# Kernel tuning notes

Measured on AMD Instinct MI355X. Metric: run time of the kernel, lower is better.

## Reference

```python
import jax, jax.numpy as jnp
import numpy as np

GAMMA = 0.9
NUM_HEADS = 8
SCALE_BASE = 512.0
GN_EPS = 1e-5


def xpos(x):
    # Canonical RetNet XPOS rotary embedding (offset=0, downscale=False).
    B, S, D = x.shape
    half = D // 2
    scale_vec = (jnp.arange(0, D, 2, dtype=jnp.float32) + 0.4 * D) / (1.4 * D)  # [half]
    power = jnp.arange(S, dtype=jnp.float32) / SCALE_BASE                        # [S]
    scale = scale_vec[None, :] ** power[:, None]                                 # [S, half]
    inv_freq = 1.0 / (10000.0 ** (jnp.arange(half, dtype=jnp.float32) / half))
    sinusoid = jnp.arange(S, dtype=jnp.float32)[:, None] * inv_freq[None, :]     # [S, half]
    sin_s = jnp.repeat(jnp.sin(sinusoid) * scale, 2, axis=-1)                    # [S, D]
    cos_s = jnp.repeat(jnp.cos(sinusoid) * scale, 2, axis=-1)
    x1, x2 = x[..., ::2], x[..., 1::2]
    rot = jnp.stack([-x2, x1], axis=-1).reshape(x.shape)  # rotate_every_two
    return x * cos_s[None] + rot * sin_s[None]


def group_norm(x, weight, bias, num_groups):
    # x: [N, C], GroupNorm over groups of channels per sample.
    N, C = x.shape
    xg = x.reshape(N, num_groups, C // num_groups)
    mu = jnp.mean(xg, axis=-1, keepdims=True)
    var = jnp.var(xg, axis=-1, keepdims=True)
    xn = ((xg - mu) * jax.lax.rsqrt(var + GN_EPS)).reshape(N, C)
    return xn * weight[None, :] + bias[None, :]


def decay_matrix(S):
    n = jnp.arange(S, dtype=jnp.float32)[:, None]
    m = jnp.arange(S, dtype=jnp.float32)[None, :]
    return jnp.where(n >= m, GAMMA ** (n - m), 0.0)  # [S, S]


def setup_inputs() -> dict:
    key = jax.random.key(0)
    ks = jax.random.split(key, 6)
    B, S, Din, Dm = 2, 2048, 512, 512
    s = 1.0 / np.sqrt(Din)
    return {
        "X": jax.random.normal(ks[0], (B, S, Din), dtype=jnp.float32),
        "Wq": jax.random.uniform(ks[1], (Din, Dm), jnp.float32, -s, s),
        "Wk": jax.random.uniform(ks[2], (Din, Dm), jnp.float32, -s, s),
        "Wv": jax.random.uniform(ks[3], (Din, Dm), jnp.float32, -s, s),
        "gn_weight": jnp.ones((Dm,), jnp.float32),
        "gn_bias": jnp.zeros((Dm,), jnp.float32),
    }


def reference(X, Wq, Wk, Wv, gn_weight, gn_bias):
    B, S, Din = X.shape
    Dm = Wq.shape[1]
    H = NUM_HEADS
    hd = Dm // H

    q = xpos(X @ Wq)                       # [B, S, Dm]
    k = xpos(X @ Wk)
    k = group_norm(k.reshape(-1, Dm), gn_weight, gn_bias, H).reshape(B, S, Dm)
    v = X @ Wv

    # [B, H, S, hd]
    q = q.reshape(B, S, H, hd).transpose(0, 2, 1, 3)
    k = k.reshape(B, S, H, hd).transpose(0, 2, 1, 3)
    v = v.reshape(B, S, H, hd).transpose(0, 2, 1, 3)

    q = q * jax.nn.sigmoid(q)              # swish-gated queries
    scores = jnp.einsum("bhsd,bhtd->bhst", q, k)  # no scale (use_scale=False)
    msr = scores * decay_matrix(S)[None, None]    # causal decay mask
    out = jnp.einsum("bhst,bhtd->bhsd", msr, v)

    out = out.transpose(0, 2, 1, 3).reshape(B, S, Dm)
    out = out + X                           # residual (input_dim == MSR_dim -> identity)
    return jax.nn.relu(out)
```

## Files before the change

kernel.cpp:

```cpp
#include <hip/hip_runtime.h>
#include <hip/hip_bf16.h>
#include <math.h>

#define NB 2
#define SEQ 2048
#define DMODEL 512
#define NH 8
#define HDIM 64
#define NROWS (NB*SEQ)
#define HALF 256
#define NT 3

typedef __attribute__((ext_vector_type(8))) short short8;
typedef __attribute__((ext_vector_type(4))) float f32x4;
typedef __attribute__((ext_vector_type(8))) unsigned short ushort8_t;

__device__ __forceinline__ unsigned short f2bf(float f) {
  union { float f; unsigned u; } v; v.f = f;
  unsigned r = v.u + 0x7fffu + ((v.u >> 16) & 1u);
  return (unsigned short)(r >> 16);
}
__device__ __forceinline__ float bf2f(unsigned short h) {
  union { unsigned u; float f; } v; v.u = ((unsigned)h) << 16;
  return v.f;
}

__device__ __forceinline__ void gload16(const void* g, void* l) {
  __builtin_amdgcn_global_load_lds(
      (const __attribute__((address_space(1))) unsigned int*)g,
      (__attribute__((address_space(3))) unsigned int*)l, 16, 0, 0);
}

__global__ __launch_bounds__(256) void k_prep(
    const float* __restrict__ X, const float* __restrict__ Wq,
    const float* __restrict__ Wk, const float* __restrict__ Wv,
    float2* __restrict__ tab, unsigned short* __restrict__ Xb,
    unsigned short* __restrict__ Wtq, unsigned short* __restrict__ Wtk,
    unsigned short* __restrict__ Wtv) {
  __shared__ float lds[64][65];
  int blk = blockIdx.x, t = threadIdx.x;
  if (blk < 512) {
    int base = (blk * 256 + t) * 4;
    int s = base >> 8, i0 = base & 255;
    float ps = (float)s * (1.0f / 512.0f);
    float fs = (float)s;
    float2 o[4];
    for (int u = 0; u < 4; ++u) {
      int i = i0 + u;
      float sv = (2.0f * (float)i + 204.8f) * (1.0f / 716.8f);
      float scale = exp2f(ps * __log2f(sv));
      float inv_freq = exp2f((float)i * (-13.287712379549449f / 256.0f));
      float theta = fs * inv_freq;
      o[u] = make_float2(__sinf(theta) * scale, __cosf(theta) * scale);
    }
    *(float4*)&tab[base]     = make_float4(o[0].x, o[0].y, o[1].x, o[1].y);
    *(float4*)&tab[base + 2] = make_float4(o[2].x, o[2].y, o[3].x, o[3].y);
  } else if (blk < 2560) {
    int base = ((blk - 512) * 256 + t) * 4;
    float4 v = *(const float4*)(X + base);
    ushort4 o;
    o.x = f2bf(v.x); o.y = f2bf(v.y); o.z = f2bf(v.z); o.w = f2bf(v.w);
    *(ushort4*)(Xb + base) = o;
  } else {
    int wb = blk - 2560;
    int which = wb >> 6;
    const float* W = which == 0 ? Wq : which == 1 ? Wk : Wv;
    unsigned short* Wt = which == 0 ? Wtq : which == 1 ? Wtk : Wtv;
    int tile = wb & 63;
    int tk = tile & 7, tn = tile >> 3;
    int k0 = tk * 64, n0 = tn * 64;
    for (int j = 0; j < 16; ++j) {
      int e = t + 256 * j;
      int r = e >> 6, c = e & 63;
      lds[r][c] = W[(size_t)(k0 + r) * DMODEL + (n0 + c)];
    }
    __syncthreads();
    for (int j = 0; j < 16; ++j) {
      int e = t + 256 * j;
      int r = e >> 6, c = e & 63;
      Wt[(size_t)(n0 + r) * DMODEL + (k0 + c)] = f2bf(lds[c][r]);
    }
  }
}

#define BM 128
#define BN 128
#define BK 64
#define KSTEPS (DMODEL / BK)
__global__ __launch_bounds__(256) void k_gemm(
    const unsigned short* __restrict__ A,
    const unsigned short* __restrict__ Btq, const unsigned short* __restrict__ Btk,
    const unsigned short* __restrict__ Btv,
    unsigned short* __restrict__ outq, unsigned short* __restrict__ outk,
    unsigned short* __restrict__ outvt) {
  int z = blockIdx.z;
  const unsigned short* Bt = (z == 0) ? Btq : (z == 1) ? Btk : Btv;
  __shared__ unsigned short Alds[2][BM * BK];
  __shared__ unsigned short Blds[2][BN * BK];
  int m0 = blockIdx.y * BM, n0 = blockIdx.x * BN;
  int t = threadIdx.x, lane = t & 63, w = t >> 6;
  int wr = w >> 1, wc = w & 1;
  f32x4 acc[4][4] = {};

  for (int j = 0; j < 4; ++j) {
    int chunk = w * 256 + j * 64 + lane;
    int r = chunk >> 3, cl = chunk & 7, cg = cl ^ (r & 7);
    gload16(&A[(size_t)(m0 + r) * DMODEL + cg * 8], &Alds[0][(w * 256 + j * 64) * 8]);
    gload16(&Bt[(size_t)(n0 + r) * DMODEL + cg * 8], &Blds[0][(w * 256 + j * 64) * 8]);
  }
  __syncthreads();
  int cur = 0;
  for (int ks = 0; ks < KSTEPS; ++ks) {
    if (ks + 1 < KSTEPS) {
      int k0 = (ks + 1) * BK;
      for (int j = 0; j < 4; ++j) {
        int chunk = w * 256 + j * 64 + lane;
        int r = chunk >> 3, cl = chunk & 7, cg = cl ^ (r & 7);
        gload16(&A[(size_t)(m0 + r) * DMODEL + k0 + cg * 8],
                &Alds[cur ^ 1][(w * 256 + j * 64) * 8]);
        gload16(&Bt[(size_t)(n0 + r) * DMODEL + k0 + cg * 8],
                &Blds[cur ^ 1][(w * 256 + j * 64) * 8]);
      }
    }
    for (int kk = 0; kk < 2; ++kk) {
      int ch = kk * 4 + (lane >> 4);
      short8 af[4], bfr[4];
      for (int mf = 0; mf < 4; ++mf) {
        int row = wr * 64 + mf * 16 + (lane & 15);
        af[mf] = *(const short8*)&Alds[cur][row * 64 + ((ch ^ (row & 7)) * 8)];
      }
      for (int nf = 0; nf < 4; ++nf) {
        int row = wc * 64 + nf * 16 + (lane & 15);
        bfr[nf] = *(const short8*)&Blds[cur][row * 64 + ((ch ^ (row & 7)) * 8)];
      }
      for (int mf = 0; mf < 4; ++mf)
        for (int nf = 0; nf < 4; ++nf)
          acc[mf][nf] = __builtin_amdgcn_mfma_f32_16x16x32_bf16(af[mf], bfr[nf], acc[mf][nf], 0, 0, 0);
    }
    __syncthreads();
    cur ^= 1;
  }
  if (z < 2) {
    unsigned short* out = (z == 0) ? outq : outk;
    for (int mf = 0; mf < 4; ++mf)
      for (int nf = 0; nf < 4; ++nf)
        for (int j = 0; j < 4; ++j) {
          int m = m0 + wr * 64 + mf * 16 + (lane >> 4) * 4 + j;
          int n = n0 + wc * 64 + nf * 16 + (lane & 15);
          out[(size_t)m * DMODEL + n] = f2bf(acc[mf][nf][j]);
        }
  } else {
    for (int mf = 0; mf < 4; ++mf)
      for (int nf = 0; nf < 4; ++nf) {
        int m = m0 + wr * 64 + mf * 16 + (lane >> 4) * 4;
        int n = n0 + wc * 64 + nf * 16 + (lane & 15);
        int b = m >> 11, s = m & (SEQ - 1);
        int h = n >> 6, d = n & 63;
        ushort4 pk;
        pk.x = f2bf(acc[mf][nf][0]); pk.y = f2bf(acc[mf][nf][1]);
        pk.z = f2bf(acc[mf][nf][2]); pk.w = f2bf(acc[mf][nf][3]);
        *(ushort4*)&outvt[((size_t)((b * NH + h) * HDIM + d)) * SEQ + s] = pk;
      }
  }
}

__global__ __launch_bounds__(256) void k_qk_transform(
    unsigned short* __restrict__ qb, unsigned short* __restrict__ kb,
    const float2* __restrict__ tab,
    const float* __restrict__ gnw, const float* __restrict__ gnb) {
  int lane = threadIdx.x & 63;
  int w = threadIdx.x >> 6;
  int row = blockIdx.x * 4 + w;
  int isk = blockIdx.y;
  unsigned short* buf = isk ? kb : qb;
  int s = row & (SEQ - 1);
  size_t off = (size_t)row * DMODEL + lane * 8;
  ushort8_t raw = *(const ushort8_t*)&buf[off];
  float v[8], r[8];
  for (int j = 0; j < 8; ++j) v[j] = bf2f(raw[j]);
  float4 t0 = *(const float4*)&tab[s * HALF + lane * 4];
  float4 t1 = *(const float4*)&tab[s * HALF + lane * 4 + 2];
  float sn[4] = {t0.x, t0.z, t1.x, t1.z};
  float cs[4] = {t0.y, t0.w, t1.y, t1.w};
  for (int p = 0; p < 4; ++p) {
    float x1 = v[2 * p], x2 = v[2 * p + 1];
    r[2 * p]     = x1 * cs[p] - x2 * sn[p];
    r[2 * p + 1] = x2 * cs[p] + x1 * sn[p];
  }
  if (!isk) {
    for (int j = 0; j < 8; ++j) r[j] = r[j] / (1.0f + __expf(-r[j]));
  } else {
    float sum = 0.0f, sq = 0.0f;
    for (int j = 0; j < 8; ++j) { sum += r[j]; sq += r[j] * r[j]; }
    for (int m = 1; m < 8; m <<= 1) { sum += __shfl_xor(sum, m); sq += __shfl_xor(sq, m); }
    float mu = sum * (1.0f / 64.0f);
    float var = sq * (1.0f / 64.0f) - mu * mu;
    float rstd = rsqrtf(var + 1e-5f);
    float4 w0 = *(const float4*)&gnw[lane * 8];
    float4 w1 = *(const float4*)&gnw[lane * 8 + 4];
    float4 b0 = *(const float4*)&gnb[lane * 8];
    float4 b1 = *(const float4*)&gnb[lane * 8 + 4];
    float wv[8] = {w0.x, w0.y, w0.z, w0.w, w1.x, w1.y, w1.z, w1.w};
    float bv[8] = {b0.x, b0.y, b0.z, b0.w, b1.x, b1.y, b1.z, b1.w};
    for (int j = 0; j < 8; ++j) r[j] = (r[j] - mu) * rstd * wv[j] + bv[j];
  }
  ushort8_t o;
  for (int j = 0; j < 8; ++j) o[j] = f2bf(r[j]);
  *(ushort8_t*)&buf[off] = o;
}

__global__ __launch_bounds__(256) void k_attn(
    const unsigned short* __restrict__ q, const unsigned short* __restrict__ k,
    const unsigned short* __restrict__ vt, const float* __restrict__ X,
    float* __restrict__ out) {
  __shared__ unsigned short klds[NT][64 * 64];
  __shared__ unsigned short vlds[NT][64 * 64];
  __shared__ unsigned short plds[4][16][72];
  int qt = blockIdx.x;
  int bh = blockIdx.y;
  int b = bh >> 3, h = bh & 7;
  int t = threadIdx.x, lane = t & 63, w = t >> 6;
  int n0 = qt * 64;
  int nw = n0 + w * 16;
  int g = lane >> 4;
  const float log2g = -0.15200309344504997f;
  short8 aq[2];
  for (int kk = 0; kk < 2; ++kk) {
    size_t off = ((size_t)(b * SEQ + nw + (lane & 15))) * DMODEL + h * HDIM + kk * 32 + g * 8;
    aq[kk] = *(const short8*)&q[off];
  }
  int kt_lo = qt - (NT - 1); if (kt_lo < 0) kt_lo = 0;
  int ntiles = qt - kt_lo + 1;
  for (int tt = 0; tt < ntiles; ++tt) {
    int m0 = (kt_lo + tt) * 64;
    for (int j = 0; j < 2; ++j) {
      int chunk = w * 128 + j * 64 + lane;
      int r = chunk >> 3, cl = chunk & 7, cg = cl ^ (r & 7);
      gload16(&k[((size_t)(b * SEQ + m0 + r)) * DMODEL + h * HDIM + cg * 8],
              &klds[tt][(w * 128 + j * 64) * 8]);
      gload16(&vt[((size_t)((b * NH + h) * HDIM + r)) * SEQ + m0 + cg * 8],
              &vlds[tt][(w * 128 + j * 64) * 8]);
    }
  }
  float xr[4][4];
  for (int nf = 0; nf < 4; ++nf)
    for (int j = 0; j < 4; ++j) {
      int srow = nw + g * 4 + j;
      int col = h * HDIM + nf * 16 + (lane & 15);
      xr[nf][j] = X[((size_t)(b * SEQ + srow)) * DMODEL + col];
    }
  float sk[4];
  for (int nf = 0; nf < 4; ++nf)
    sk[nf] = exp2f(-(float)(nf * 16 + (lane & 15)) * log2g);
  int nrb = nw + g * 4;
  f32x4 o[4] = {};
  __syncthreads();
  for (int tt = 0; tt < ntiles; ++tt) {
    int m0 = (kt_lo + tt) * 64;
    float sq_[4];
    for (int j = 0; j < 4; ++j)
      sq_[j] = exp2f((float)(nrb + j - m0) * log2g);
    f32x4 sc[4] = {};
    for (int kk = 0; kk < 2; ++kk) {
      int ch = kk * 4 + g;
      for (int nf = 0; nf < 4; ++nf) {
        int row = nf * 16 + (lane & 15);
        short8 bk = *(const short8*)&klds[tt][row * 64 + ((ch ^ (row & 7)) * 8)];
        sc[nf] = __builtin_amdgcn_mfma_f32_16x16x32_bf16(aq[kk], bk, sc[nf], 0, 0, 0);
      }
    }
    for (int nf = 0; nf < 4; ++nf) {
      int cin = nf * 16 + (lane & 15);
      for (int j = 0; j < 4; ++j) {
        int dlt = nrb + j - (m0 + cin);
        float f = (dlt >= 0) ? sq_[j] * sk[nf] : 0.0f;
        plds[w][g * 4 + j][cin] = f2bf(sc[nf][j] * f);
      }
    }
    for (int kk = 0; kk < 2; ++kk) {
      int ch = kk * 4 + g;
      short8 pa = *(const short8*)&plds[w][lane & 15][kk * 32 + g * 8];
      for (int nf = 0; nf < 4; ++nf) {
        int row = nf * 16 + (lane & 15);
        short8 bv = *(const short8*)&vlds[tt][row * 64 + ((ch ^ (row & 7)) * 8)];
        o[nf] = __builtin_amdgcn_mfma_f32_16x16x32_bf16(pa, bv, o[nf], 0, 0, 0);
      }
    }
  }
  for (int nf = 0; nf < 4; ++nf)
    for (int j = 0; j < 4; ++j) {
      int srow = nw + g * 4 + j;
      int col = h * HDIM + nf * 16 + (lane & 15);
      size_t off = ((size_t)(b * SEQ + srow)) * DMODEL + col;
      float val = o[nf][j] + xr[nf][j];
      out[off] = val > 0.0f ? val : 0.0f;
    }
}

extern "C" void kernel_launch(void* const* d_in, const int* in_sizes, int n_in,
                              void* d_out, int out_size, void* d_ws, size_t ws_size,
                              hipStream_t stream) {
  const float* X   = (const float*)d_in[0];
  const float* Wq  = (const float*)d_in[1];
  const float* Wk  = (const float*)d_in[2];
  const float* Wv  = (const float*)d_in[3];
  const float* gnw = (const float*)d_in[4];
  const float* gnb = (const float*)d_in[5];
  float* out = (float*)d_out;
  char* ws = (char*)d_ws;

  float2*         tab  = (float2*)ws;
  unsigned short* Xb   = (unsigned short*)(ws + (4u << 20));
  unsigned short* Wtq  = (unsigned short*)(ws + (8u << 20));
  unsigned short* Wtk  = Wtq + 512 * 512;
  unsigned short* Wtv  = Wtk + 512 * 512;
  unsigned short* qb   = (unsigned short*)(ws + (8u << 20) + 3u * 512 * 512 * 2);
  unsigned short* kb   = qb + (size_t)NROWS * DMODEL;
  unsigned short* vt   = kb + (size_t)NROWS * DMODEL;

  k_prep<<<dim3(2752), dim3(256), 0, stream>>>(X, Wq, Wk, Wv, tab, Xb, Wtq, Wtk, Wtv);
  k_gemm<<<dim3(4, 32, 3), dim3(256), 0, stream>>>(Xb, Wtq, Wtk, Wtv, qb, kb, vt);
  k_qk_transform<<<dim3(1024, 2), dim3(256), 0, stream>>>(qb, kb, tab, gnw, gnb);
  k_attn<<<dim3(32, 16), dim3(256), 0, stream>>>(qb, kb, vt, X, out);
}
```

Before: 40.52 us.

## Fuse four kernels into one cooperative persistent kernel with grid syncs

Replaces the prep, QKV GEMM, q/k transform and attention launches with a single cooperative kernel of 256 blocks of 512 threads, separated by grid.sync barriers. The GEMM is retiled to 64x128 tiles and loops over the three weight matrices per block, and attention processes two query tiles per block, one per half-block. The goal is to remove per-launch overhead and inter-kernel gaps. In exchange it adds grid-wide barrier cost, lower parallelism in the GEMM phase, and a large static shared-memory footprint that limits occupancy.

```diff
diff --git a/kernel.cpp b/kernel.cpp
--- a/kernel.cpp
+++ b/kernel.cpp
@@ -1,5 +1,6 @@
 #include <hip/hip_runtime.h>
 #include <hip/hip_bf16.h>
+#include <hip/hip_cooperative_groups.h>
 #include <math.h>
 
 #define NB 2
@@ -10,6 +11,8 @@
 #define NROWS (NB*SEQ)
 #define HALF 256
 #define NT 3
+#define BK 64
+#define KSTEPS (DMODEL / BK)
 
 typedef __attribute__((ext_vector_type(8))) short short8;
 typedef __attribute__((ext_vector_type(4))) float f32x4;
@@ -31,270 +34,280 @@
       (__attribute__((address_space(3))) unsigned int*)l, 16, 0, 0);
 }
 
-__global__ __launch_bounds__(256) void k_prep(
+#define SMEM_BYTES 116736
+
+__global__ __launch_bounds__(512, 2) void k_fused(
     const float* __restrict__ X, const float* __restrict__ Wq,
     const float* __restrict__ Wk, const float* __restrict__ Wv,
+    const float* __restrict__ gnw, const float* __restrict__ gnb,
     float2* __restrict__ tab, unsigned short* __restrict__ Xb,
     unsigned short* __restrict__ Wtq, unsigned short* __restrict__ Wtk,
-    unsigned short* __restrict__ Wtv) {
-  __shared__ float lds[64][65];
-  int blk = blockIdx.x, t = threadIdx.x;
-  if (blk < 512) {
-    int base = (blk * 256 + t) * 4;
-    int s = base >> 8, i0 = base & 255;
-    float ps = (float)s * (1.0f / 512.0f);
-    float fs = (float)s;
-    float2 o[4];
-    for (int u = 0; u < 4; ++u) {
-      int i = i0 + u;
-      float sv = (2.0f * (float)i + 204.8f) * (1.0f / 716.8f);
-      float scale = exp2f(ps * __log2f(sv));
-      float inv_freq = exp2f((float)i * (-13.287712379549449f / 256.0f));
-      float theta = fs * inv_freq;
-      o[u] = make_float2(__sinf(theta) * scale, __cosf(theta) * scale);
-    }
-    *(float4*)&tab[base]     = make_float4(o[0].x, o[0].y, o[1].x, o[1].y);
-    *(float4*)&tab[base + 2] = make_float4(o[2].x, o[2].y, o[3].x, o[3].y);
-  } else if (blk < 2560) {
-    int base = ((blk - 512) * 256 + t) * 4;
-    float4 v = *(const float4*)(X + base);
-    ushort4 o;
-    o.x = f2bf(v.x); o.y = f2bf(v.y); o.z = f2bf(v.z); o.w = f2bf(v.w);
-    *(ushort4*)(Xb + base) = o;
-  } else {
-    int wb = blk - 2560;
-    int which = wb >> 6;
-    const float* W = which == 0 ? Wq : which == 1 ? Wk : Wv;
-    unsigned short* Wt = which == 0 ? Wtq : which == 1 ? Wtk : Wtv;
-    int tile = wb & 63;
-    int tk = tile & 7, tn = tile >> 3;
-    int k0 = tk * 64, n0 = tn * 64;
-    for (int j = 0; j < 16; ++j) {
-      int e = t + 256 * j;
-      int r = e >> 6, c = e & 63;
-      lds[r][c] = W[(size_t)(k0 + r) * DMODEL + (n0 + c)];
-    }
+    unsigned short* __restrict__ Wtv,
+    unsigned short* __restrict__ qb, unsigned short* __restrict__ kb,
+    unsigned short* __restrict__ vt, float* __restrict__ out) {
+  __shared__ __align__(16) char smem[SMEM_BYTES];
+  cooperative_groups::grid_group grid = cooperative_groups::this_grid();
+  int bid = blockIdx.x, t = threadIdx.x;
+  int lane = t & 63;
+  const float log2g = -0.15200309344504997f;
+
+  {
+    int gtid = bid * 512 + t;
+    {
+      int base = gtid * 4;
+      int s = base >> 8, i0 = base & 255;
+      float ps = (float)s * (1.0f / 512.0f);
+      float fs = (float)s;
+      float2 o[4];
+      for (int u = 0; u < 4; ++u) {
+        int i = i0 + u;
+        float sv = (2.0f * (float)i + 204.8f) * (1.0f / 716.8f);
+        float scale = exp2f(ps * __log2f(sv));
+        float inv_freq = exp2f((float)i * (-13.287712379549449f / 256.0f));
+        float theta = fs * inv_freq;
+        o[u] = make_float2(__sinf(theta) * scale, __cosf(theta) * scale);
+      }
+      *(float4*)&tab[base]     = make_float4(o[0].x, o[0].y, o[1].x, o[1].y);
+      *(float4*)&tab[base + 2] = make_float4(o[2].x, o[2].y, o[3].x, o[3].y);
+    }
+    for (int it = 0; it < 4; ++it) {
+      int base = (it * 131072 + gtid) * 4;
+      float4 v = *(const float4*)(X + base);
+      ushort4 o;
+      o.x = f2bf(v.x); o.y = f2bf(v.y); o.z = f2bf(v.z); o.w = f2bf(v.w);
+      *(ushort4*)(Xb + base) = o;
+    }
+    if (bid < 192) {
+      float (*lds)[65] = (float (*)[65])smem;
+      int which = bid >> 6;
+      const float* W = which == 0 ? Wq : which == 1 ? Wk : Wv;
+      unsigned short* Wt = which == 0 ? Wtq : which == 1 ? Wtk : Wtv;
+      int tile = bid & 63;
+      int tk = tile & 7, tn = tile >> 3;
+      int k0 = tk * 64, n0 = tn * 64;
+      for (int j = 0; j < 8; ++j) {
+        int e = t + 512 * j;
+        int r = e >> 6, c = e & 63;
+        lds[r][c] = W[(size_t)(k0 + r) * DMODEL + (n0 + c)];
+      }
+      __syncthreads();
+      for (int j = 0; j < 8; ++j) {
+        int e = t + 512 * j;
+        int r = e >> 6, c = e & 63;
+        Wt[(size_t)(n0 + r) * DMODEL + (k0 + c)] = f2bf(lds[c][r]);
+      }
+    }
+  }
+  grid.sync();
+
+  {
+    unsigned short* Alds = (unsigned short*)smem;
+    unsigned short* Blds = (unsigned short*)(smem + 16384);
+    int w = t >> 6;
+    int wr = w >> 2, wc = w & 3;
+    int m0 = (bid >> 2) * 64, n0 = (bid & 3) * 128;
+    for (int z = 0; z < 3; ++z) {
+      const unsigned short* Bt = (z == 0) ? Wtq : (z == 1) ? Wtk : Wtv;
+      f32x4 acc[2][2] = {};
+      {
+        int chunk = w * 64 + lane;
+        int r = chunk >> 3, cl = chunk & 7, cg = cl ^ (r & 7);
+        gload16(&Xb[(size_t)(m0 + r) * DMODEL + cg * 8], &Alds[w * 512]);
+        for (int j = 0; j < 2; ++j) {
+          int chb = w * 128 + j * 64 + lane;
+          int rb = chb >> 3, clb = chb & 7, cgb = clb ^ (rb & 7);
+          gload16(&Bt[(size_t)(n0 + rb) * DMODEL + cgb * 8], &Blds[w * 1024 + j * 512]);
+        }
+      }
+      __syncthreads();
+      int cur = 0;
+      for (int ks = 0; ks < KSTEPS; ++ks) {
+        if (ks + 1 < KSTEPS) {
+          int k0 = (ks + 1) * BK;
+          int chunk = w * 64 + lane;
+          int r = chunk >> 3, cl = chunk & 7, cg = cl ^ (r & 7);
+          gload16(&Xb[(size_t)(m0 + r) * DMODEL + k0 + cg * 8],
+                  &Alds[(cur ^ 1) * 4096 + w * 512]);
+          for (int j = 0; j < 2; ++j) {
+            int chb = w * 128 + j * 64 + lane;
+            int rb = chb >> 3, clb = chb & 7, cgb = clb ^ (rb & 7);
+            gload16(&Bt[(size_t)(n0 + rb) * DMODEL + k0 + cgb * 8],
+                    &Blds[(cur ^ 1) * 8192 + w * 1024 + j * 512]);
+          }
+        }
+        for (int kk = 0; kk < 2; ++kk) {
+          int ch = kk * 4 + (lane >> 4);
+          short8 af[2], bfr[2];
+          for (int mf = 0; mf < 2; ++mf) {
+            int row = wr * 32 + mf * 16 + (lane & 15);
+            af[mf] = *(const short8*)&Alds[cur * 4096 + row * 64 + ((ch ^ (row & 7)) * 8)];
+          }
+          for (int nf = 0; nf < 2; ++nf) {
+            int row = wc * 32 + nf * 16 + (lane & 15);
+            bfr[nf] = *(const short8*)&Blds[cur * 8192 + row * 64 + ((ch ^ (row & 7)) * 8)];
+          }
+          for (int mf = 0; mf < 2; ++mf)
+            for (int nf = 0; nf < 2; ++nf)
+              acc[mf][nf] = __builtin_amdgcn_mfma_f32_16x16x32_bf16(af[mf], bfr[nf], acc[mf][nf], 0, 0, 0);
+        }
+        __syncthreads();
+        cur ^= 1;
+      }
+      int g = lane >> 4;
+      if (z < 2) {
+        unsigned short* o = (z == 0) ? qb : kb;
+        for (int mf = 0; mf < 2; ++mf)
+          for (int nf = 0; nf < 2; ++nf)
+            for (int j = 0; j < 4; ++j) {
+              int m = m0 + wr * 32 + mf * 16 + g * 4 + j;
+              int n = n0 + wc * 32 + nf * 16 + (lane & 15);
+              o[(size_t)m * DMODEL + n] = f2bf(acc[mf][nf][j]);
+            }
+      } else {
+        for (int mf = 0; mf < 2; ++mf)
+          for (int nf = 0; nf < 2; ++nf) {
+            int m = m0 + wr * 32 + mf * 16 + g * 4;
+            int n = n0 + wc * 32 + nf * 16 + (lane & 15);
+            int b = m >> 11, s = m & (SEQ - 1);
+            int h = n >> 6, d = n & 63;
+            ushort4 pk;
+            pk.x = f2bf(acc[mf][nf][0]); pk.y = f2bf(acc[mf][nf][1]);
+            pk.z = f2bf(acc[mf][nf][2]); pk.w = f2bf(acc[mf][nf][3]);
+            *(ushort4*)&vt[((size_t)((b * NH + h) * HDIM + d)) * SEQ + s] = pk;
+          }
+      }
+    }
+  }
+  grid.sync();
+
+  for (int it = 0; it < 4; ++it) {
+    int ru = it * 2048 + bid * 8 + (t >> 6);
+    int isk = ru >> 12;
+    int row = ru & 4095;
+    unsigned short* buf = isk ? kb : qb;
+    int s = row & (SEQ - 1);
+    size_t off = (size_t)row * DMODEL + lane * 8;
+    ushort8_t raw = *(const ushort8_t*)&buf[off];
+    float v[8], r[8];
+    for (int j = 0; j < 8; ++j) v[j] = bf2f(raw[j]);
+    float4 t0 = *(const float4*)&tab[s * HALF + lane * 4];
+    float4 t1 = *(const float4*)&tab[s * HALF + lane * 4 + 2];
+    float sn[4] = {t0.x, t0.z, t1.x, t1.z};
+    float cs[4] = {t0.y, t0.w, t1.y, t1.w};
+    for (int p = 0; p < 4; ++p) {
+      float x1 = v[2 * p], x2 = v[2 * p + 1];
+      r[2 * p]     = x1 * cs[p] - x2 * sn[p];
+      r[2 * p + 1] = x2 * cs[p] + x1 * sn[p];
+    }
+    if (!isk) {
+      for (int j = 0; j < 8; ++j) r[j] = r[j] / (1.0f + __expf(-r[j]));
+    } else {
+      float sum = 0.0f, sq = 0.0f;
+      for (int j = 0; j < 8; ++j) { sum += r[j]; sq += r[j] * r[j]; }
+      for (int m = 1; m < 8; m <<= 1) { sum += __shfl_xor(sum, m); sq += __shfl_xor(sq, m); }
+      float mu = sum * (1.0f / 64.0f);
+      float var = sq * (1.0f / 64.0f) - mu * mu;
+      float rstd = rsqrtf(var + 1e-5f);
+      float4 w0 = *(const float4*)&gnw[lane * 8];
+      float4 w1 = *(const float4*)&gnw[lane * 8 + 4];
+      float4 b0 = *(const float4*)&gnb[lane * 8];
+      float4 b1 = *(const float4*)&gnb[lane * 8 + 4];
+      float wv[8] = {w0.x, w0.y, w0.z, w0.w, w1.x, w1.y, w1.z, w1.w};
+      float bv[8] = {b0.x, b0.y, b0.z, b0.w, b1.x, b1.y, b1.z, b1.w};
+      for (int j = 0; j < 8; ++j) r[j] = (r[j] - mu) * rstd * wv[j] + bv[j];
+    }
+    ushort8_t o;
+    for (int j = 0; j < 8; ++j) o[j] = f2bf(r[j]);
+    *(ushort8_t*)&buf[off] = o;
+  }
+  grid.sync();
+
+  {
+    int half = t >> 8;
+    int t2 = t & 255;
+    int w2 = t2 >> 6;
+    int unit = bid * 2 + half;
+    int qt = unit & 31, bh = unit >> 5;
+    int b = bh >> 3, h = bh & 7;
+    char* sb = smem + half * 58368;
+    unsigned short* klds = (unsigned short*)sb;
+    unsigned short* vlds = (unsigned short*)(sb + 24576);
+    unsigned short* pbase = (unsigned short*)(sb + 49152);
+    int n0 = qt * 64;
+    int nw = n0 + w2 * 16;
+    int g = lane >> 4;
+    short8 aq[2];
+    for (int kk = 0; kk < 2; ++kk) {
+      size_t off = ((size_t)(b * SEQ + nw + (lane & 15))) * DMODEL + h * HDIM + kk * 32 + g * 8;
+      aq[kk] = *(const short8*)&qb[off];
+    }
+    int kt_lo = qt - (NT - 1); if (kt_lo < 0) kt_lo = 0;
+    int ntiles = qt - kt_lo + 1;
+    for (int tt = 0; tt < ntiles; ++tt) {
+      int m0 = (kt_lo + tt) * 64;
+      for (int j = 0; j < 2; ++j) {
+        int chunk = w2 * 128 + j * 64 + lane;
+        int r = chunk >> 3, cl = chunk & 7, cg = cl ^ (r & 7);
+        gload16(&kb[((size_t)(b * SEQ + m0 + r)) * DMODEL + h * HDIM + cg * 8],
+                &klds[tt * 4096 + w2 * 1024 + j * 512]);
+        gload16(&vt[((size_t)((b * NH + h) * HDIM + r)) * SEQ + m0 + cg * 8],
+                &vlds[tt * 4096 + w2 * 1024 + j * 512]);
+      }
+    }
+    float xr[4][4];
+    for (int nf = 0; nf < 4; ++nf)
+      for (int j = 0; j < 4; ++j) {
+        int srow = nw + g * 4 + j;
+        int col = h * HDIM + nf * 16 + (lane & 15);
+        xr[nf][j] = X[((size_t)(b * SEQ + srow)) * DMODEL + col];
+      }
+    float sk[4];
+    for (int nf = 0; nf < 4; ++nf)
+      sk[nf] = exp2f(-(float)(nf * 16 + (lane & 15)) * log2g);
+    int nrb = nw + g * 4;
+    f32x4 o[4] = {};
     __syncthreads();
-    for (int j = 0; j < 16; ++j) {
-      int e = t + 256 * j;
-      int r = e >> 6, c = e & 63;
-      Wt[(size_t)(n0 + r) * DMODEL + (k0 + c)] = f2bf(lds[c][r]);
-    }
+    for (int tt = 0; tt < ntiles; ++tt) {
+      int m0 = (kt_lo + tt) * 64;
+      float sq_[4];
+      for (int j = 0; j < 4; ++j)
+        sq_[j] = exp2f((float)(nrb + j - m0) * log2g);
+      f32x4 sc[4] = {};
+      for (int kk = 0; kk < 2; ++kk) {
+        int ch = kk * 4 + g;
+        for (int nf = 0; nf < 4; ++nf) {
+          int row = nf * 16 + (lane & 15);
+          short8 bk = *(const short8*)&klds[tt * 4096 + row * 64 + ((ch ^ (row & 7)) * 8)];
+          sc[nf] = __builtin_amdgcn_mfma_f32_16x16x32_bf16(aq[kk], bk, sc[nf], 0, 0, 0);
+        }
+      }
+      for (int nf = 0; nf < 4; ++nf) {
+        int cin = nf * 16 + (lane & 15);
+        for (int j = 0; j < 4; ++j) {
+          int dlt = nrb + j - (m0 + cin);
+          float f = (dlt >= 0) ? sq_[j] * sk[nf] : 0.0f;
+          pbase[w2 * 1152 + (g * 4 + j) * 72 + cin] = f2bf(sc[nf][j] * f);
+        }
+      }
+      for (int kk = 0; kk < 2; ++kk) {
+        int ch = kk * 4 + g;
+        short8 pa = *(const short8*)&pbase[w2 * 1152 + (lane & 15) * 72 + kk * 32 + g * 8];
+        for (int nf = 0; nf < 4; ++nf) {
+          int row = nf * 16 + (lane & 15);
+          short8 bv = *(const short8*)&vlds[tt * 4096 + row * 64 + ((ch ^ (row & 7)) * 8)];
+          o[nf] = __builtin_amdgcn_mfma_f32_16x16x32_bf16(pa, bv, o[nf], 0, 0, 0);
+        }
+      }
+    }
+    for (int nf = 0; nf < 4; ++nf)
+      for (int j = 0; j < 4; ++j) {
+        int srow = nw + g * 4 + j;
+        int col = h * HDIM + nf * 16 + (lane & 15);
+        size_t off = ((size_t)(b * SEQ + srow)) * DMODEL + col;
+        float val = o[nf][j] + xr[nf][j];
+        out[off] = val > 0.0f ? val : 0.0f;
+      }
   }
-}
-
-#define BM 128
-#define BN 128
-#define BK 64
-#define KSTEPS (DMODEL / BK)
-__global__ __launch_bounds__(256) void k_gemm(
-    const unsigned short* __restrict__ A,
-    const unsigned short* __restrict__ Btq, const unsigned short* __restrict__ Btk,
-    const unsigned short* __restrict__ Btv,
-    unsigned short* __restrict__ outq, unsigned short* __restrict__ outk,
-    unsigned short* __restrict__ outvt) {
-  int z = blockIdx.z;
-  const unsigned short* Bt = (z == 0) ? Btq : (z == 1) ? Btk : Btv;
-  __shared__ unsigned short Alds[2][BM * BK];
-  __shared__ unsigned short Blds[2][BN * BK];
-  int m0 = blockIdx.y * BM, n0 = blockIdx.x * BN;
-  int t = threadIdx.x, lane = t & 63, w = t >> 6;
-  int wr = w >> 1, wc = w & 1;
-  f32x4 acc[4][4] = {};
-
-  for (int j = 0; j < 4; ++j) {
-    int chunk = w * 256 + j * 64 + lane;
-    int r = chunk >> 3, cl = chunk & 7, cg = cl ^ (r & 7);
-    gload16(&A[(size_t)(m0 + r) * DMODEL + cg * 8], &Alds[0][(w * 256 + j * 64) * 8]);
-    gload16(&Bt[(size_t)(n0 + r) * DMODEL + cg * 8], &Blds[0][(w * 256 + j * 64) * 8]);
-  }
-  __syncthreads();
-  int cur = 0;
-  for (int ks = 0; ks < KSTEPS; ++ks) {
-    if (ks + 1 < KSTEPS) {
-      int k0 = (ks + 1) * BK;
-      for (int j = 0; j < 4; ++j) {
-        int chunk = w * 256 + j * 64 + lane;
-        int r = chunk >> 3, cl = chunk & 7, cg = cl ^ (r & 7);
-        gload16(&A[(size_t)(m0 + r) * DMODEL + k0 + cg * 8],
-                &Alds[cur ^ 1][(w * 256 + j * 64) * 8]);
-        gload16(&Bt[(size_t)(n0 + r) * DMODEL + k0 + cg * 8],
-                &Blds[cur ^ 1][(w * 256 + j * 64) * 8]);
-      }
-    }
-    for (int kk = 0; kk < 2; ++kk) {
-      int ch = kk * 4 + (lane >> 4);
-      short8 af[4], bfr[4];
-      for (int mf = 0; mf < 4; ++mf) {
-        int row = wr * 64 + mf * 16 + (lane & 15);
-        af[mf] = *(const short8*)&Alds[cur][row * 64 + ((ch ^ (row & 7)) * 8)];
-      }
-      for (int nf = 0; nf < 4; ++nf) {
-        int row = wc * 64 + nf * 16 + (lane & 15);
-        bfr[nf] = *(const short8*)&Blds[cur][row * 64 + ((ch ^ (row & 7)) * 8)];
-      }
-      for (int mf = 0; mf < 4; ++mf)
-        for (int nf = 0; nf < 4; ++nf)
-          acc[mf][nf] = __builtin_amdgcn_mfma_f32_16x16x32_bf16(af[mf], bfr[nf], acc[mf][nf], 0, 0, 0);
-    }
-    __syncthreads();
-    cur ^= 1;
-  }
-  if (z < 2) {
-    unsigned short* out = (z == 0) ? outq : outk;
-    for (int mf = 0; mf < 4; ++mf)
-      for (int nf = 0; nf < 4; ++nf)
-        for (int j = 0; j < 4; ++j) {
-          int m = m0 + wr * 64 + mf * 16 + (lane >> 4) * 4 + j;
-          int n = n0 + wc * 64 + nf * 16 + (lane & 15);
-          out[(size_t)m * DMODEL + n] = f2bf(acc[mf][nf][j]);
-        }
-  } else {
-    for (int mf = 0; mf < 4; ++mf)
-      for (int nf = 0; nf < 4; ++nf) {
-        int m = m0 + wr * 64 + mf * 16 + (lane >> 4) * 4;
-        int n = n0 + wc * 64 + nf * 16 + (lane & 15);
-        int b = m >> 11, s = m & (SEQ - 1);
-        int h = n >> 6, d = n & 63;
-        ushort4 pk;
-        pk.x = f2bf(acc[mf][nf][0]); pk.y = f2bf(acc[mf][nf][1]);
-        pk.z = f2bf(acc[mf][nf][2]); pk.w = f2bf(acc[mf][nf][3]);
-        *(ushort4*)&outvt[((size_t)((b * NH + h) * HDIM + d)) * SEQ + s] = pk;
-      }
-  }
-}
-
-__global__ __launch_bounds__(256) void k_qk_transform(
-    unsigned short* __restrict__ qb, unsigned short* __restrict__ kb,
-    const float2* __restrict__ tab,
-    const float* __restrict__ gnw, const float* __restrict__ gnb) {
-  int lane = threadIdx.x & 63;
-  int w = threadIdx.x >> 6;
-  int row = blockIdx.x * 4 + w;
-  int isk = blockIdx.y;
-  unsigned short* buf = isk ? kb : qb;
-  int s = row & (SEQ - 1);
-  size_t off = (size_t)row * DMODEL + lane * 8;
-  ushort8_t raw = *(const ushort8_t*)&buf[off];
-  float v[8], r[8];
-  for (int j = 0; j < 8; ++j) v[j] = bf2f(raw[j]);
-  float4 t0 = *(const float4*)&tab[s * HALF + lane * 4];
-  float4 t1 = *(const float4*)&tab[s * HALF + lane * 4 + 2];
-  float sn[4] = {t0.x, t0.z, t1.x, t1.z};
-  float cs[4] = {t0.y, t0.w, t1.y, t1.w};
-  for (int p = 0; p < 4; ++p) {
-    float x1 = v[2 * p], x2 = v[2 * p + 1];
-    r[2 * p]     = x1 * cs[p] - x2 * sn[p];
-    r[2 * p + 1] = x2 * cs[p] + x1 * sn[p];
-  }
-  if (!isk) {
-    for (int j = 0; j < 8; ++j) r[j] = r[j] / (1.0f + __expf(-r[j]));
-  } else {
-    float sum = 0.0f, sq = 0.0f;
-    for (int j = 0; j < 8; ++j) { sum += r[j]; sq += r[j] * r[j]; }
-    for (int m = 1; m < 8; m <<= 1) { sum += __shfl_xor(sum, m); sq += __shfl_xor(sq, m); }
-    float mu = sum * (1.0f / 64.0f);
-    float var = sq * (1.0f / 64.0f) - mu * mu;
-    float rstd = rsqrtf(var + 1e-5f);
-    float4 w0 = *(const float4*)&gnw[lane * 8];
-    float4 w1 = *(const float4*)&gnw[lane * 8 + 4];
-    float4 b0 = *(const float4*)&gnb[lane * 8];
-    float4 b1 = *(const float4*)&gnb[lane * 8 + 4];
-    float wv[8] = {w0.x, w0.y, w0.z, w0.w, w1.x, w1.y, w1.z, w1.w};
-    float bv[8] = {b0.x, b0.y, b0.z, b0.w, b1.x, b1.y, b1.z, b1.w};
-    for (int j = 0; j < 8; ++j) r[j] = (r[j] - mu) * rstd * wv[j] + bv[j];
-  }
-  ushort8_t o;
-  for (int j = 0; j < 8; ++j) o[j] = f2bf(r[j]);
-  *(ushort8_t*)&buf[off] = o;
-}
-
-__global__ __launch_bounds__(256) void k_attn(
-    const unsigned short* __restrict__ q, const unsigned short* __restrict__ k,
-    const unsigned short* __restrict__ vt, const float* __restrict__ X,
-    float* __restrict__ out) {
-  __shared__ unsigned short klds[NT][64 * 64];
-  __shared__ unsigned short vlds[NT][64 * 64];
-  __shared__ unsigned short plds[4][16][72];
-  int qt = blockIdx.x;
-  int bh = blockIdx.y;
-  int b = bh >> 3, h = bh & 7;
-  int t = threadIdx.x, lane = t & 63, w = t >> 6;
-  int n0 = qt * 64;
-  int nw = n0 + w * 16;
-  int g = lane >> 4;
-  const float log2g = -0.15200309344504997f;
-  short8 aq[2];
-  for (int kk = 0; kk < 2; ++kk) {
-    size_t off = ((size_t)(b * SEQ + nw + (lane & 15))) * DMODEL + h * HDIM + kk * 32 + g * 8;
-    aq[kk] = *(const short8*)&q[off];
-  }
-  int kt_lo = qt - (NT - 1); if (kt_lo < 0) kt_lo = 0;
-  int ntiles = qt - kt_lo + 1;
-  for (int tt = 0; tt < ntiles; ++tt) {
-    int m0 = (kt_lo + tt) * 64;
-    for (int j = 0; j < 2; ++j) {
-      int chunk = w * 128 + j * 64 + lane;
-      int r = chunk >> 3, cl = chunk & 7, cg = cl ^ (r & 7);
-      gload16(&k[((size_t)(b * SEQ + m0 + r)) * DMODEL + h * HDIM + cg * 8],
-              &klds[tt][(w * 128 + j * 64) * 8]);
-      gload16(&vt[((size_t)((b * NH + h) * HDIM + r)) * SEQ + m0 + cg * 8],
-              &vlds[tt][(w * 128 + j * 64) * 8]);
-    }
-  }
-  float xr[4][4];
-  for (int nf = 0; nf < 4; ++nf)
-    for (int j = 0; j < 4; ++j) {
-      int srow = nw + g * 4 + j;
-      int col = h * HDIM + nf * 16 + (lane & 15);
-      xr[nf][j] = X[((size_t)(b * SEQ + srow)) * DMODEL + col];
-    }
-  float sk[4];
-  for (int nf = 0; nf < 4; ++nf)
-    sk[nf] = exp2f(-(float)(nf * 16 + (lane & 15)) * log2g);
-  int nrb = nw + g * 4;
-  f32x4 o[4] = {};
-  __syncthreads();
-  for (int tt = 0; tt < ntiles; ++tt) {
-    int m0 = (kt_lo + tt) * 64;
-    float sq_[4];
-    for (int j = 0; j < 4; ++j)
-      sq_[j] = exp2f((float)(nrb + j - m0) * log2g);
-    f32x4 sc[4] = {};
-    for (int kk = 0; kk < 2; ++kk) {
-      int ch = kk * 4 + g;
-      for (int nf = 0; nf < 4; ++nf) {
-        int row = nf * 16 + (lane & 15);
-        short8 bk = *(const short8*)&klds[tt][row * 64 + ((ch ^ (row & 7)) * 8)];
-        sc[nf] = __builtin_amdgcn_mfma_f32_16x16x32_bf16(aq[kk], bk, sc[nf], 0, 0, 0);
-      }
-    }
-    for (int nf = 0; nf < 4; ++nf) {
-      int cin = nf * 16 + (lane & 15);
-      for (int j = 0; j < 4; ++j) {
-        int dlt = nrb + j - (m0 + cin);
-        float f = (dlt >= 0) ? sq_[j] * sk[nf] : 0.0f;
-        plds[w][g * 4 + j][cin] = f2bf(sc[nf][j] * f);
-      }
-    }
-    for (int kk = 0; kk < 2; ++kk) {
-      int ch = kk * 4 + g;
-      short8 pa = *(const short8*)&plds[w][lane & 15][kk * 32 + g * 8];
-      for (int nf = 0; nf < 4; ++nf) {
-        int row = nf * 16 + (lane & 15);
-        short8 bv = *(const short8*)&vlds[tt][row * 64 + ((ch ^ (row & 7)) * 8)];
-        o[nf] = __builtin_amdgcn_mfma_f32_16x16x32_bf16(pa, bv, o[nf], 0, 0, 0);
-      }
-    }
-  }
-  for (int nf = 0; nf < 4; ++nf)
-    for (int j = 0; j < 4; ++j) {
-      int srow = nw + g * 4 + j;
-      int col = h * HDIM + nf * 16 + (lane & 15);
-      size_t off = ((size_t)(b * SEQ + srow)) * DMODEL + col;
-      float val = o[nf][j] + xr[nf][j];
-      out[off] = val > 0.0f ? val : 0.0f;
-    }
 }
 
 extern "C" void kernel_launch(void* const* d_in, const int* in_sizes, int n_in,
@@ -318,8 +331,7 @@
   unsigned short* kb   = qb + (size_t)NROWS * DMODEL;
   unsigned short* vt   = kb + (size_t)NROWS * DMODEL;
 
-  k_prep<<<dim3(2752), dim3(256), 0, stream>>>(X, Wq, Wk, Wv, tab, Xb, Wtq, Wtk, Wtv);
-  k_gemm<<<dim3(4, 32, 3), dim3(256), 0, stream>>>(Xb, Wtq, Wtk, Wtv, qb, kb, vt);
-  k_qk_transform<<<dim3(1024, 2), dim3(256), 0, stream>>>(qb, kb, tab, gnw, gnb);
-  k_attn<<<dim3(32, 16), dim3(256), 0, stream>>>(qb, kb, vt, X, out);
-}
+  void* args[] = {&X, &Wq, &Wk, &Wv, &gnw, &gnb, &tab, &Xb, &Wtq, &Wtk, &Wtv,
+                  &qb, &kb, &vt, &out};
+  hipLaunchCooperativeKernel((void*)k_fused, dim3(256), dim3(512), args, 0, stream);
+}
```

New measurement: 148.2 us. +265.8%, slower.
